# Kernel optimization log

Hardware: AMD Instinct MI355X
Metric: run time of the kernel (lower is better)

The kernel has to match this reference:

```python
import jax, jax.numpy as jnp
import numpy as np

D_MODEL, D_STATE, EXPAND = 1024, 256, 2
BATCH, SEQ = 8, 2048


def setup_inputs() -> dict:
    key = jax.random.key(0)
    ks = jax.random.split(key, 7)
    s = 0.02
    return {
        "x": jax.random.normal(ks[0], (BATCH, SEQ, D_MODEL), jnp.float32),
        "W_in": jax.random.normal(ks[1], (D_MODEL, D_MODEL * EXPAND), jnp.float32) * s,
        "b_in": jax.random.normal(ks[2], (D_MODEL * EXPAND,), jnp.float32) * s,
        "W_state": jax.random.normal(ks[3], (D_MODEL * EXPAND, D_STATE), jnp.float32) * s,
        "b_state": jax.random.normal(ks[4], (D_STATE,), jnp.float32) * s,
        "W_out": jax.random.normal(ks[5], (D_STATE, D_MODEL), jnp.float32) * s,
        "b_out": jax.random.normal(ks[6], (D_MODEL,), jnp.float32) * s,
        "init_state": jnp.zeros((1, D_STATE), jnp.float32),
    }


def reference(x, W_in, b_in, W_state, b_state, W_out, b_out, init_state):
    # x: [B, T, D]
    x_proj = jax.nn.silu(jnp.einsum("btd,de->bte", x, W_in) + b_in)  # [B,T,2D]
    # state_proj depends only on x_proj, so batch the GEMM over all timesteps
    updates = jnp.einsum("bte,es->bts", x_proj, W_state) + b_state    # [B,T,S]
    updates_t = jnp.swapaxes(updates, 0, 1)                            # [T,B,S]
    state0 = jnp.broadcast_to(init_state, (x.shape[0], init_state.shape[1]))

    def step(state, u):
        new = jax.nn.silu(state + u)
        return new, new

    _, states = jax.lax.scan(step, state0, updates_t)  # [T,B,S]
    out = jnp.einsum("tbs,sd->tbd", states, W_out) + b_out  # [T,B,D]
    return jnp.swapaxes(out, 0, 1)  # [B,T,D]
```

## Files before the change

### kernel.cpp

```cpp
#include <hip/hip_runtime.h>
#include <cstdint>
#include <cstddef>

#define BATCH 8
#define SEQ   2048
#define DM    1024
#define DE    2048
#define DSZ   256
#define MROWS (BATCH*SEQ)
#define MCHUNK 8192

typedef _Float16 f16;
typedef _Float16 f16x4 __attribute__((ext_vector_type(4)));
typedef _Float16 f16x8 __attribute__((ext_vector_type(8)));
typedef float  f32x4  __attribute__((ext_vector_type(4)));

__device__ __forceinline__ void glds16(const void* gp, void* lp) {
  __builtin_amdgcn_global_load_lds(
      (const __attribute__((address_space(1))) void*)gp,
      (__attribute__((address_space(3))) void*)lp, 16, 0, 0);
}

__device__ __forceinline__ float silu_f(float x) {
  return x * __builtin_amdgcn_rcpf(1.0f + __expf(-x));
}

__device__ __forceinline__ int swz(int k8, int r) { return k8 ^ ((r >> 1) & 3); }

__global__ void split_x_k(const float* __restrict__ in, f16* __restrict__ oh,
                          f16* __restrict__ ol, int n) {
  int i = (blockIdx.x * blockDim.x + threadIdx.x) * 4;
  const int stride = gridDim.x * blockDim.x * 4;
  for (; i < n; i += stride) {
    float4 v = *(const float4*)(in + i);
    f16x4 h, l;
    h[0] = (f16)v.x; l[0] = (f16)(v.x - (float)h[0]);
    h[1] = (f16)v.y; l[1] = (f16)(v.y - (float)h[1]);
    h[2] = (f16)v.z; l[2] = (f16)(v.z - (float)h[2]);
    h[3] = (f16)v.w; l[3] = (f16)(v.w - (float)h[3]);
    *(f16x4*)(oh + i) = h;
    *(f16x4*)(ol + i) = l;
  }
}

__global__ void transpose_split_k(const float* __restrict__ in, f16* __restrict__ oh,
                                  f16* __restrict__ ol, int R, int C) {
  __shared__ float tile[32][33];
  const int c0 = blockIdx.x * 32, r0 = blockIdx.y * 32;
  const int tx = threadIdx.x, ty = threadIdx.y;
  #pragma unroll
  for (int i = 0; i < 4; ++i)
    tile[ty + i*8][tx] = in[(size_t)(r0 + ty + i*8) * C + c0 + tx];
  __syncthreads();
  #pragma unroll
  for (int i = 0; i < 4; ++i) {
    float v = tile[tx][ty + i*8];
    f16 h = (f16)v;
    size_t idx = (size_t)(c0 + ty + i*8) * R + r0 + tx;
    oh[idx] = h;
    ol[idx] = (f16)(v - (float)h);
  }
}

__global__ void transpose_cast_f16_k(const float* __restrict__ in, f16* __restrict__ out, int R, int C) {
  __shared__ float tile[32][33];
  const int c0 = blockIdx.x * 32, r0 = blockIdx.y * 32;
  const int tx = threadIdx.x, ty = threadIdx.y;
  #pragma unroll
  for (int i = 0; i < 4; ++i)
    tile[ty + i*8][tx] = in[(size_t)(r0 + ty + i*8) * C + c0 + tx];
  __syncthreads();
  #pragma unroll
  for (int i = 0; i < 4; ++i)
    out[(size_t)(c0 + ty + i*8) * R + r0 + tx] = (f16)tile[tx][ty + i*8];
}

__global__ __launch_bounds__(512) void gemm1_k(const f16* __restrict__ Ah, const f16* __restrict__ Al,
                                               const f16* __restrict__ Bh, const f16* __restrict__ Bl,
                                               const float* __restrict__ bias,
                                               f16* __restrict__ Ch, f16* __restrict__ Cl) {
  const int K = 1024, N = 2048;
  __shared__ f16 sAh[2][4096], sAl[2][4096], sBh[2][4096], sBl[2][4096];

  const int tid = threadIdx.x;
  const int w = tid >> 6, l = tid & 63;
  const int bid = blockIdx.x;
  const int xcd = bid & 7, loc = bid >> 3;
  const int mt = xcd * 8 + (loc & 7);
  const int nt = loc >> 3;
  const int bm = mt * 128, bn = nt * 128;
  const int wm = (w >> 2) * 64, wn = (w & 3) * 32;
  const int lr = l & 15, lq = l >> 4;

  const int r = tid >> 2, k8 = swz(tid & 3, r);
  const f16* pAh = Ah + (size_t)(bm + r) * K + k8 * 8;
  const f16* pAl = Al + (size_t)(bm + r) * K + k8 * 8;
  const f16* pBh = Bh + (size_t)(bn + r) * K + k8 * 8;
  const f16* pBl = Bl + (size_t)(bn + r) * K + k8 * 8;
  const int dst = tid * 8;

  int offA[4], offB[2];
  #pragma unroll
  for (int i = 0; i < 4; ++i) {
    const int row = wm + i*16 + lr;
    offA[i] = row * 32 + swz(lq, row) * 8;
  }
  #pragma unroll
  for (int j = 0; j < 2; ++j) {
    const int row = wn + j*16 + lr;
    offB[j] = row * 32 + swz(lq, row) * 8;
  }

  f32x4 acc[4][2] = {};

  glds16(pAh, &sAh[0][dst]); glds16(pAl, &sAl[0][dst]);
  glds16(pBh, &sBh[0][dst]); glds16(pBl, &sBl[0][dst]);
  pAh += 32; pAl += 32; pBh += 32; pBl += 32;
  __syncthreads();

  for (int kt = 0; kt < 32; ++kt) {
    const int cur = kt & 1;
    if (kt < 31) {
      const int nxt = cur ^ 1;
      glds16(pAh, &sAh[nxt][dst]); glds16(pAl, &sAl[nxt][dst]);
      glds16(pBh, &sBh[nxt][dst]); glds16(pBl, &sBl[nxt][dst]);
      pAh += 32; pAl += 32; pBh += 32; pBl += 32;
    }
    f16x8 ah[4], al[4], bh[2], bl[2];
    #pragma unroll
    for (int i = 0; i < 4; ++i) {
      ah[i] = *(const f16x8*)(&sAh[cur][0] + offA[i]);
      al[i] = *(const f16x8*)(&sAl[cur][0] + offA[i]);
    }
    #pragma unroll
    for (int j = 0; j < 2; ++j) {
      bh[j] = *(const f16x8*)(&sBh[cur][0] + offB[j]);
      bl[j] = *(const f16x8*)(&sBl[cur][0] + offB[j]);
    }
    __builtin_amdgcn_s_setprio(1);
    #pragma unroll
    for (int i = 0; i < 4; ++i)
      #pragma unroll
      for (int j = 0; j < 2; ++j) {
        acc[i][j] = __builtin_amdgcn_mfma_f32_16x16x32_f16(ah[i], bh[j], acc[i][j], 0, 0, 0);
        acc[i][j] = __builtin_amdgcn_mfma_f32_16x16x32_f16(ah[i], bl[j], acc[i][j], 0, 0, 0);
        acc[i][j] = __builtin_amdgcn_mfma_f32_16x16x32_f16(al[i], bh[j], acc[i][j], 0, 0, 0);
      }
    __builtin_amdgcn_s_setprio(0);
    __syncthreads();
  }

  #pragma unroll
  for (int j = 0; j < 2; ++j) {
    const int col = bn + wn + j*16 + lr;
    const float bv = bias[col];
    #pragma unroll
    for (int i = 0; i < 4; ++i)
      #pragma unroll
      for (int r4 = 0; r4 < 4; ++r4) {
        const int row = bm + wm + i*16 + lq*4 + r4;
        const float s = silu_f(acc[i][j][r4] + bv);
        const f16 h = (f16)s;
        const size_t idx = (size_t)row * N + col;
        Ch[idx] = h;
        Cl[idx] = (f16)(s - (float)h);
      }
  }
}

__global__ __launch_bounds__(512) void gemm2s_k(const f16* __restrict__ Ah, const f16* __restrict__ Al,
                                                const f16* __restrict__ Bh, const f16* __restrict__ Bl,
                                                const float* __restrict__ bias,
                                                float* __restrict__ C) {
  const int K = 2048, N = 256;
  __shared__ f16 sAh[2][2][2048], sAl[2][2][2048], sBh[2][2][2048], sBl[2][2][2048];

  const int tid = threadIdx.x;
  const int w = tid >> 6, l = tid & 63;
  const int bid = blockIdx.x;
  const int bm = (bid & 127) * 64;
  const int bn = (bid >> 7) * 64;
  const int wm = (w >> 1) * 16, wn = (w & 1) * 32;
  const int lr = l & 15, lq = l >> 4;

  const int c = tid & 255, s = tid >> 8;
  const int r = c >> 2, k8 = swz(c & 3, r);
  const size_t koff = (size_t)s * 32 + k8 * 8;
  const f16* pAh = Ah + (size_t)(bm + r) * K + koff;
  const f16* pAl = Al + (size_t)(bm + r) * K + koff;
  const f16* pBh = Bh + (size_t)(bn + r) * K + koff;
  const f16* pBl = Bl + (size_t)(bn + r) * K + koff;
  const int dst = c * 8;

  int offA, offB[2];
  {
    const int row = wm + lr;
    offA = row * 32 + swz(lq, row) * 8;
  }
  #pragma unroll
  for (int j = 0; j < 2; ++j) {
    const int row = wn + j*16 + lr;
    offB[j] = row * 32 + swz(lq, row) * 8;
  }

  f32x4 acc[2] = {};

  glds16(pAh, &sAh[0][s][dst]); glds16(pAl, &sAl[0][s][dst]);
  glds16(pBh, &sBh[0][s][dst]); glds16(pBl, &sBl[0][s][dst]);
  pAh += 64; pAl += 64; pBh += 64; pBl += 64;
  __syncthreads();

  for (int kt = 0; kt < 32; ++kt) {
    const int cur = kt & 1;
    if (kt < 31) {
      const int nxt = cur ^ 1;
      glds16(pAh, &sAh[nxt][s][dst]); glds16(pAl, &sAl[nxt][s][dst]);
      glds16(pBh, &sBh[nxt][s][dst]); glds16(pBl, &sBl[nxt][s][dst]);
      pAh += 64; pAl += 64; pBh += 64; pBl += 64;
    }
    #pragma unroll
    for (int ss = 0; ss < 2; ++ss) {
      f16x8 ah, al, bh[2], bl[2];
      ah = *(const f16x8*)(&sAh[cur][ss][0] + offA);
      al = *(const f16x8*)(&sAl[cur][ss][0] + offA);
      #pragma unroll
      for (int j = 0; j < 2; ++j) {
        bh[j] = *(const f16x8*)(&sBh[cur][ss][0] + offB[j]);
        bl[j] = *(const f16x8*)(&sBl[cur][ss][0] + offB[j]);
      }
      __builtin_amdgcn_s_setprio(1);
      #pragma unroll
      for (int j = 0; j < 2; ++j) {
        acc[j] = __builtin_amdgcn_mfma_f32_16x16x32_f16(ah, bh[j], acc[j], 0, 0, 0);
        acc[j] = __builtin_amdgcn_mfma_f32_16x16x32_f16(ah, bl[j], acc[j], 0, 0, 0);
        acc[j] = __builtin_amdgcn_mfma_f32_16x16x32_f16(al, bh[j], acc[j], 0, 0, 0);
      }
      __builtin_amdgcn_s_setprio(0);
    }
    __syncthreads();
  }

  #pragma unroll
  for (int j = 0; j < 2; ++j) {
    const int col = bn + wn + j*16 + lr;
    const float bv = bias[col];
    #pragma unroll
    for (int r4 = 0; r4 < 4; ++r4) {
      const int row = bm + wm + lq*4 + r4;
      C[(size_t)row * N + col] = acc[j][r4] + bv;
    }
  }
}

__global__ __launch_bounds__(256) void gemm3_k(const f16* __restrict__ A,
                                               const f16* __restrict__ Bt,
                                               const float* __restrict__ bias,
                                               float* __restrict__ C) {
  const int K = 256, N = 1024;
  __shared__ f16 sA[2][4096], sB[2][4096];

  const int tid = threadIdx.x;
  const int w = tid >> 6, l = tid & 63;
  const int bm = blockIdx.y * 128, bn = blockIdx.x * 128;
  const int wm = (w >> 1) * 64, wn = (w & 1) * 64;
  const int lr = l & 15, lq = l >> 4;

  const f16 *pA[2], *pB[2]; int dstc[2];
  #pragma unroll
  for (int p = 0; p < 2; ++p) {
    const int c = p * 256 + tid;
    const int r = c >> 2, k8 = swz(c & 3, r);
    pA[p] = A  + (size_t)(bm + r) * K + k8 * 8;
    pB[p] = Bt + (size_t)(bn + r) * K + k8 * 8;
    dstc[p] = c * 8;
  }

  int offA[4], offB[4];
  #pragma unroll
  for (int i = 0; i < 4; ++i) {
    const int rowA = wm + i*16 + lr;
    const int rowB = wn + i*16 + lr;
    offA[i] = rowA * 32 + swz(lq, rowA) * 8;
    offB[i] = rowB * 32 + swz(lq, rowB) * 8;
  }

  f32x4 acc[4][4] = {};

  glds16(pA[0], &sA[0][dstc[0]]); glds16(pA[1], &sA[0][dstc[1]]);
  glds16(pB[0], &sB[0][dstc[0]]); glds16(pB[1], &sB[0][dstc[1]]);
  pA[0] += 32; pA[1] += 32; pB[0] += 32; pB[1] += 32;
  __syncthreads();

  for (int kt = 0; kt < 8; ++kt) {
    const int cur = kt & 1;
    if (kt < 7) {
      const int nxt = cur ^ 1;
      glds16(pA[0], &sA[nxt][dstc[0]]); glds16(pA[1], &sA[nxt][dstc[1]]);
      glds16(pB[0], &sB[nxt][dstc[0]]); glds16(pB[1], &sB[nxt][dstc[1]]);
      pA[0] += 32; pA[1] += 32; pB[0] += 32; pB[1] += 32;
    }
    f16x8 af[4], bfr[4];
    #pragma unroll
    for (int i = 0; i < 4; ++i) af[i]  = *(const f16x8*)(&sA[cur][0] + offA[i]);
    #pragma unroll
    for (int j = 0; j < 4; ++j) bfr[j] = *(const f16x8*)(&sB[cur][0] + offB[j]);
    __builtin_amdgcn_s_setprio(1);
    #pragma unroll
    for (int i = 0; i < 4; ++i)
      #pragma unroll
      for (int j = 0; j < 4; ++j)
        acc[i][j] = __builtin_amdgcn_mfma_f32_16x16x32_f16(af[i], bfr[j], acc[i][j], 0, 0, 0);
    __builtin_amdgcn_s_setprio(0);
    __syncthreads();
  }

  #pragma unroll
  for (int j = 0; j < 4; ++j) {
    const int col = bn + wn + j*16 + lr;
    const float bv = bias[col];
    #pragma unroll
    for (int i = 0; i < 4; ++i)
      #pragma unroll
      for (int r4 = 0; r4 < 4; ++r4) {
        const int row = bm + wm + i*16 + lq*4 + r4;
        C[(size_t)row * N + col] = acc[i][j][r4] + bv;
      }
  }
}

#define L2E 1.4426950408889634f
__global__ __launch_bounds__(64) void scan_k(const float* __restrict__ upd,
                                             const float* __restrict__ init,
                                             f16* __restrict__ states) {
  const int b = blockIdx.x >> 2, sq = blockIdx.x & 3;
  const int s = sq * 64 + threadIdx.x;
  const float* u = upd + (size_t)b * SEQ * DSZ + s;
  f16* st = states + (size_t)b * SEQ * DSZ + s;
  float state = init[s];

  float r0[16], r1[16], r2[16], ulog[16];
  #pragma unroll
  for (int i = 0; i < 16; ++i) r0[i] = u[(size_t)i * DSZ];
  #pragma unroll
  for (int i = 0; i < 16; ++i) r1[i] = u[(size_t)(16 + i) * DSZ];
  #pragma unroll
  for (int i = 0; i < 16; ++i) ulog[i] = r0[i] * (-L2E);

  for (int t0 = 0; t0 < SEQ; t0 += 16) {
    if (t0 + 32 < SEQ) {
      #pragma unroll
      for (int i = 0; i < 16; ++i) r2[i] = u[(size_t)(t0 + 32 + i) * DSZ];
    }
    f16 res[16];
    #pragma unroll
    for (int i = 0; i < 16; ++i) {
      const float e = __builtin_amdgcn_exp2f(__builtin_fmaf(state, -L2E, ulog[i]));
      const float x = state + r0[i];
      state = x * __builtin_amdgcn_rcpf(1.0f + e);
      res[i] = (f16)state;
    }
    #pragma unroll
    for (int i = 0; i < 16; ++i) st[(size_t)(t0 + i) * DSZ] = res[i];
    #pragma unroll
    for (int i = 0; i < 16; ++i) { r0[i] = r1[i]; ulog[i] = r1[i] * (-L2E); r1[i] = r2[i]; }
  }
}

extern "C" void kernel_launch(void* const* d_in, const int* in_sizes, int n_in,
                              void* d_out, int out_size, void* d_ws, size_t ws_size,
                              hipStream_t stream) {
  const float* x       = (const float*)d_in[0];
  const float* W_in    = (const float*)d_in[1];
  const float* b_in    = (const float*)d_in[2];
  const float* W_state = (const float*)d_in[3];
  const float* b_state = (const float*)d_in[4];
  const float* W_out   = (const float*)d_in[5];
  const float* b_out   = (const float*)d_in[6];
  const float* init_st = (const float*)d_in[7];
  float* out = (float*)d_out;

  char* ws = (char*)d_ws;
  f16*   xh        = (f16*)(ws + 0);
  f16*   xl        = (f16*)(ws + 33554432);
  f16*   xproj_h   = (f16*)(ws + 67108864);
  f16*   xproj_l   = (f16*)(ws + 100663296);
  float* upd       = (float*)(ws + 134217728);
  f16*   states    = (f16*)(ws + 150994944);
  f16*   w_in_h    = (f16*)(ws + 159383552);
  f16*   w_in_l    = (f16*)(ws + 163577856);
  f16*   w_state_h = (f16*)(ws + 167772160);
  f16*   w_state_l = (f16*)(ws + 168820736);
  f16*   w_out_t   = (f16*)(ws + 169869312);

  split_x_k<<<4096, 256, 0, stream>>>(x, xh, xl, MROWS * DM);
  dim3 tb(32, 8);
  transpose_split_k<<<dim3(DE/32,  DM/32), tb, 0, stream>>>(W_in,    w_in_h,    w_in_l,    DM,  DE);
  transpose_split_k<<<dim3(DSZ/32, DE/32), tb, 0, stream>>>(W_state, w_state_h, w_state_l, DE,  DSZ);
  transpose_cast_f16_k<<<dim3(DM/32, DSZ/32), tb, 0, stream>>>(W_out, w_out_t, DSZ, DM);

  for (int c = 0; c < 2; ++c) {
    const size_t ro = (size_t)c * MCHUNK;
    gemm1_k<<<1024, 512, 0, stream>>>(
        xh + ro * DM, xl + ro * DM, w_in_h, w_in_l, b_in, xproj_h, xproj_l);
    gemm2s_k<<<512, 512, 0, stream>>>(
        xproj_h, xproj_l, w_state_h, w_state_l, b_state, upd + ro * DSZ);
  }

  scan_k<<<BATCH*4, 64, 0, stream>>>(upd, init_st, states);

  gemm3_k<<<dim3(DM/128, MROWS/128), 256, 0, stream>>>(states, w_out_t, b_out, out);
}
```

Measured before the change: 533.5 us.

## Merge prepass kernels into one launch and load gemm2 A operand directly to registers

```diff
diff --git a/kernel.cpp b/kernel.cpp
--- a/kernel.cpp
+++ b/kernel.cpp
@@ -27,27 +27,46 @@
 
 __device__ __forceinline__ int swz(int k8, int r) { return k8 ^ ((r >> 1) & 3); }
 
-__global__ void split_x_k(const float* __restrict__ in, f16* __restrict__ oh,
-                          f16* __restrict__ ol, int n) {
-  int i = (blockIdx.x * blockDim.x + threadIdx.x) * 4;
-  const int stride = gridDim.x * blockDim.x * 4;
-  for (; i < n; i += stride) {
-    float4 v = *(const float4*)(in + i);
-    f16x4 h, l;
-    h[0] = (f16)v.x; l[0] = (f16)(v.x - (float)h[0]);
-    h[1] = (f16)v.y; l[1] = (f16)(v.y - (float)h[1]);
-    h[2] = (f16)v.z; l[2] = (f16)(v.z - (float)h[2]);
-    h[3] = (f16)v.w; l[3] = (f16)(v.w - (float)h[3]);
-    *(f16x4*)(oh + i) = h;
-    *(f16x4*)(ol + i) = l;
-  }
-}
-
-__global__ void transpose_split_k(const float* __restrict__ in, f16* __restrict__ oh,
-                                  f16* __restrict__ ol, int R, int C) {
+__global__ __launch_bounds__(256) void prepass_k(
+    const float* __restrict__ x, const float* __restrict__ W_in,
+    const float* __restrict__ W_state, const float* __restrict__ W_out,
+    f16* __restrict__ xh, f16* __restrict__ xl,
+    f16* __restrict__ w_in_h, f16* __restrict__ w_in_l,
+    f16* __restrict__ w_state_h, f16* __restrict__ w_state_l,
+    f16* __restrict__ w_out_t) {
+  const int bid = blockIdx.x, tid = threadIdx.x;
+  if (bid < 4096) {
+    const int n = MROWS * DM;
+    int i = (bid * 256 + tid) * 4;
+    const int stride = 4096 * 256 * 4;
+    for (; i < n; i += stride) {
+      float4 v = *(const float4*)(x + i);
+      f16x4 h, lo;
+      h[0] = (f16)v.x; lo[0] = (f16)(v.x - (float)h[0]);
+      h[1] = (f16)v.y; lo[1] = (f16)(v.y - (float)h[1]);
+      h[2] = (f16)v.z; lo[2] = (f16)(v.z - (float)h[2]);
+      h[3] = (f16)v.w; lo[3] = (f16)(v.w - (float)h[3]);
+      *(f16x4*)(xh + i) = h;
+      *(f16x4*)(xl + i) = lo;
+    }
+    return;
+  }
   __shared__ float tile[32][33];
-  const int c0 = blockIdx.x * 32, r0 = blockIdx.y * 32;
-  const int tx = threadIdx.x, ty = threadIdx.y;
+  const int tx = tid & 31, ty = tid >> 5;
+  const float* in; f16 *oh, *ol; int R, C, c0, r0; bool split;
+  if (bid < 6144) {
+    const int id = bid - 4096;
+    in = W_in; R = DM; C = DE; c0 = (id & 63) * 32; r0 = (id >> 6) * 32;
+    oh = w_in_h; ol = w_in_l; split = true;
+  } else if (bid < 6656) {
+    const int id = bid - 6144;
+    in = W_state; R = DE; C = DSZ; c0 = (id & 7) * 32; r0 = (id >> 3) * 32;
+    oh = w_state_h; ol = w_state_l; split = true;
+  } else {
+    const int id = bid - 6656;
+    in = W_out; R = DSZ; C = DM; c0 = (id & 31) * 32; r0 = (id >> 5) * 32;
+    oh = w_out_t; ol = nullptr; split = false;
+  }
   #pragma unroll
   for (int i = 0; i < 4; ++i)
     tile[ty + i*8][tx] = in[(size_t)(r0 + ty + i*8) * C + c0 + tx];
@@ -58,21 +77,8 @@
     f16 h = (f16)v;
     size_t idx = (size_t)(c0 + ty + i*8) * R + r0 + tx;
     oh[idx] = h;
-    ol[idx] = (f16)(v - (float)h);
-  }
-}
-
-__global__ void transpose_cast_f16_k(const float* __restrict__ in, f16* __restrict__ out, int R, int C) {
-  __shared__ float tile[32][33];
-  const int c0 = blockIdx.x * 32, r0 = blockIdx.y * 32;
-  const int tx = threadIdx.x, ty = threadIdx.y;
-  #pragma unroll
-  for (int i = 0; i < 4; ++i)
-    tile[ty + i*8][tx] = in[(size_t)(r0 + ty + i*8) * C + c0 + tx];
-  __syncthreads();
-  #pragma unroll
-  for (int i = 0; i < 4; ++i)
-    out[(size_t)(c0 + ty + i*8) * R + r0 + tx] = (f16)tile[tx][ty + i*8];
+    if (split) ol[idx] = (f16)(v - (float)h);
+  }
 }
 
 __global__ __launch_bounds__(512) void gemm1_k(const f16* __restrict__ Ah, const f16* __restrict__ Al,
@@ -173,7 +179,7 @@
                                                 const float* __restrict__ bias,
                                                 float* __restrict__ C) {
   const int K = 2048, N = 256;
-  __shared__ f16 sAh[2][2][2048], sAl[2][2][2048], sBh[2][2][2048], sBl[2][2][2048];
+  __shared__ f16 sBh[2][2][2048], sBl[2][2][2048];
 
   const int tid = threadIdx.x;
   const int w = tid >> 6, l = tid & 63;
@@ -184,19 +190,14 @@
   const int lr = l & 15, lq = l >> 4;
 
   const int c = tid & 255, s = tid >> 8;
-  const int r = c >> 2, k8 = swz(c & 3, r);
-  const size_t koff = (size_t)s * 32 + k8 * 8;
-  const f16* pAh = Ah + (size_t)(bm + r) * K + koff;
-  const f16* pAl = Al + (size_t)(bm + r) * K + koff;
-  const f16* pBh = Bh + (size_t)(bn + r) * K + koff;
-  const f16* pBl = Bl + (size_t)(bn + r) * K + koff;
-  const int dst = c * 8;
-
-  int offA, offB[2];
-  {
-    const int row = wm + lr;
-    offA = row * 32 + swz(lq, row) * 8;
-  }
+  const int rB = c >> 2, k8 = swz(c & 3, rB);
+  const f16* pBh = Bh + (size_t)(bn + rB) * K + s * 32 + k8 * 8;
+  const f16* pBl = Bl + (size_t)(bn + rB) * K + s * 32 + k8 * 8;
+  const int dstB = c * 8;
+
+  const size_t arow = (size_t)(bm + wm + lr) * K + lq * 8;
+
+  int offB[2];
   #pragma unroll
   for (int j = 0; j < 2; ++j) {
     const int row = wn + j*16 + lr;
@@ -204,25 +205,28 @@
   }
 
   f32x4 acc[2] = {};
-
-  glds16(pAh, &sAh[0][s][dst]); glds16(pAl, &sAl[0][s][dst]);
-  glds16(pBh, &sBh[0][s][dst]); glds16(pBl, &sBl[0][s][dst]);
-  pAh += 64; pAl += 64; pBh += 64; pBl += 64;
+  f16x8 ahc[2], alc[2], ahn[2], aln[2];
+
+  glds16(pBh, &sBh[0][s][dstB]); glds16(pBl, &sBl[0][s][dstB]);
+  pBh += 64; pBl += 64;
+  ahc[0] = *(const f16x8*)(Ah + arow);       ahc[1] = *(const f16x8*)(Ah + arow + 32);
+  alc[0] = *(const f16x8*)(Al + arow);       alc[1] = *(const f16x8*)(Al + arow + 32);
   __syncthreads();
 
+  #pragma unroll 2
   for (int kt = 0; kt < 32; ++kt) {
     const int cur = kt & 1;
     if (kt < 31) {
       const int nxt = cur ^ 1;
-      glds16(pAh, &sAh[nxt][s][dst]); glds16(pAl, &sAl[nxt][s][dst]);
-      glds16(pBh, &sBh[nxt][s][dst]); glds16(pBl, &sBl[nxt][s][dst]);
-      pAh += 64; pAl += 64; pBh += 64; pBl += 64;
+      glds16(pBh, &sBh[nxt][s][dstB]); glds16(pBl, &sBl[nxt][s][dstB]);
+      pBh += 64; pBl += 64;
+      const size_t ko = arow + (size_t)(kt + 1) * 64;
+      ahn[0] = *(const f16x8*)(Ah + ko);     ahn[1] = *(const f16x8*)(Ah + ko + 32);
+      aln[0] = *(const f16x8*)(Al + ko);     aln[1] = *(const f16x8*)(Al + ko + 32);
     }
     #pragma unroll
     for (int ss = 0; ss < 2; ++ss) {
-      f16x8 ah, al, bh[2], bl[2];
-      ah = *(const f16x8*)(&sAh[cur][ss][0] + offA);
-      al = *(const f16x8*)(&sAl[cur][ss][0] + offA);
+      f16x8 bh[2], bl[2];
       #pragma unroll
       for (int j = 0; j < 2; ++j) {
         bh[j] = *(const f16x8*)(&sBh[cur][ss][0] + offB[j]);
@@ -231,13 +235,15 @@
       __builtin_amdgcn_s_setprio(1);
       #pragma unroll
       for (int j = 0; j < 2; ++j) {
-        acc[j] = __builtin_amdgcn_mfma_f32_16x16x32_f16(ah, bh[j], acc[j], 0, 0, 0);
-        acc[j] = __builtin_amdgcn_mfma_f32_16x16x32_f16(ah, bl[j], acc[j], 0, 0, 0);
-        acc[j] = __builtin_amdgcn_mfma_f32_16x16x32_f16(al, bh[j], acc[j], 0, 0, 0);
+        acc[j] = __builtin_amdgcn_mfma_f32_16x16x32_f16(ahc[ss], bh[j], acc[j], 0, 0, 0);
+        acc[j] = __builtin_amdgcn_mfma_f32_16x16x32_f16(ahc[ss], bl[j], acc[j], 0, 0, 0);
+        acc[j] = __builtin_amdgcn_mfma_f32_16x16x32_f16(alc[ss], bh[j], acc[j], 0, 0, 0);
       }
       __builtin_amdgcn_s_setprio(0);
     }
     __syncthreads();
+    ahc[0] = ahn[0]; ahc[1] = ahn[1];
+    alc[0] = aln[0]; alc[1] = aln[1];
   }
 
   #pragma unroll
@@ -392,11 +398,9 @@
   f16*   w_state_l = (f16*)(ws + 168820736);
   f16*   w_out_t   = (f16*)(ws + 169869312);
 
-  split_x_k<<<4096, 256, 0, stream>>>(x, xh, xl, MROWS * DM);
-  dim3 tb(32, 8);
-  transpose_split_k<<<dim3(DE/32,  DM/32), tb, 0, stream>>>(W_in,    w_in_h,    w_in_l,    DM,  DE);
-  transpose_split_k<<<dim3(DSZ/32, DE/32), tb, 0, stream>>>(W_state, w_state_h, w_state_l, DE,  DSZ);
-  transpose_cast_f16_k<<<dim3(DM/32, DSZ/32), tb, 0, stream>>>(W_out, w_out_t, DSZ, DM);
+  prepass_k<<<6912, 256, 0, stream>>>(x, W_in, W_state, W_out,
+                                      xh, xl, w_in_h, w_in_l,
+                                      w_state_h, w_state_l, w_out_t);
 
   for (int c = 0; c < 2; ++c) {
     const size_t ro = (size_t)c * MCHUNK;
```

Result: slower. 602.3 us (+12.9%).
